# Optimization experiments

Measured on AMD Instinct MI355X. Metric: run time of the kernel, lower is better.

The kernel has to match this reference:

```python
import jax, jax.numpy as jnp
import numpy as np

NUM_NODES = 500000
INPUT_DIM = 256
ATTN_DIM = 64
NUM_GRAPHS = 512


def setup_inputs() -> dict:
    key = jax.random.key(0)
    ks = jax.random.split(key, 6)
    x = jax.random.normal(ks[0], (NUM_NODES, INPUT_DIM), dtype=jnp.float32)
    batch = jnp.sort(jax.random.randint(ks[1], (NUM_NODES,), 0, NUM_GRAPHS, dtype=jnp.int32)).astype(jnp.int64)
    # Xavier-uniform style init for linear weights, normal(0, 0.1) for context
    lim1 = float(np.sqrt(6.0 / (INPUT_DIM + ATTN_DIM)))
    W_att = jax.random.uniform(ks[2], (ATTN_DIM, INPUT_DIM), minval=-lim1, maxval=lim1, dtype=jnp.float32)
    b_att = jnp.zeros((ATTN_DIM,), dtype=jnp.float32)
    ctx = 0.1 * jax.random.normal(ks[3], (ATTN_DIM,), dtype=jnp.float32)
    lim2 = float(np.sqrt(6.0 / (INPUT_DIM + INPUT_DIM)))
    W_out = jax.random.uniform(ks[4], (INPUT_DIM, INPUT_DIM), minval=-lim2, maxval=lim2, dtype=jnp.float32)
    b_out = jnp.zeros((INPUT_DIM,), dtype=jnp.float32)
    return {"x": x, "batch": batch, "W_att": W_att, "b_att": b_att, "ctx": ctx, "W_out": W_out, "b_out": b_out}


def reference(x, batch, W_att, b_att, ctx, W_out, b_out):
    seg = batch.astype(jnp.int32)
    # attention scores per node: tanh(x W^T + b) . ctx  -> [N]
    logits = jnp.tanh(x @ W_att.T + b_att)
    scores = logits @ ctx  # [N]
    # segment-wise stable softmax
    seg_max = jax.ops.segment_max(scores, seg, num_segments=NUM_GRAPHS)
    exp_s = jnp.exp(scores - seg_max[seg])
    seg_sum = jax.ops.segment_sum(exp_s, seg, num_segments=NUM_GRAPHS)
    w = exp_s / (seg_sum[seg] + 1e-8)  # [N]
    # weighted segment-sum pooling -> [B, D]
    pooled = jax.ops.segment_sum(x * w[:, None], seg, num_segments=NUM_GRAPHS)
    return pooled @ W_out.T + b_out
```

## Files before the change

### kernel.cpp

```cpp
#include <hip/hip_runtime.h>
#include <hip/hip_bf16.h>
#include <math.h>

#define N_NODES 500000
#define DIM 256
#define ADIM 64
#define NG 512
#define PSPLIT 4

typedef __attribute__((ext_vector_type(8))) short short8;
typedef __attribute__((ext_vector_type(4))) short short4v;
typedef __attribute__((ext_vector_type(4))) float floatx4;

__device__ inline unsigned short f2bf(float f) {
    union { float f; unsigned int u; } v; v.f = f;
    unsigned int u = v.u;
    unsigned int r = u + 0x7FFFu + ((u >> 16) & 1u);
    return (unsigned short)(r >> 16);
}

__global__ __launch_bounds__(256) void k_prep(const float* __restrict__ W_out,
                                              float* __restrict__ Wt_out) {
    int idx = blockIdx.x * 256 + threadIdx.x;
    if (idx < DIM * DIM) {
        int o = idx / DIM, d = idx % DIM;
        Wt_out[d * DIM + o] = W_out[idx];
    }
}

__global__ __launch_bounds__(256) void k_offsets(const int* __restrict__ batch,
                                                 int* __restrict__ seg_start) {
    int i = blockIdx.x * 256 + threadIdx.x;
    if (i >= N_NODES) return;
    int b = batch[i];
    if (i == 0) {
        for (int g = 0; g <= b; g++) seg_start[g] = 0;
    } else {
        int pb = batch[i - 1];
        if (pb != b) {
            for (int g = pb + 1; g <= b; g++) seg_start[g] = i;
        }
    }
    if (i == N_NODES - 1) {
        for (int g = b + 1; g <= NG; g++) seg_start[g] = N_NODES;
    }
}

__global__ __launch_bounds__(256) void k_scores(const float* __restrict__ x,
                                                const float* __restrict__ W_att,
                                                const float* __restrict__ b_att,
                                                const float* __restrict__ ctx,
                                                float* __restrict__ scores) {
    __shared__ __align__(16) unsigned short xs[64 * 40];
    __shared__ float sacc[4][64];

    const int t = threadIdx.x;
    const int wave = t >> 6;
    const int lane = t & 63;
    const int quad = lane >> 4;
    const int lcol = lane & 15;
    const int base = blockIdx.x * 64;

    short8 bfrag[8];
    {
        const float* wr = W_att + (size_t)(16 * wave + lcol) * DIM + quad * 8;
#pragma unroll
        for (int s = 0; s < 8; s++) {
            float4 f0 = *(const float4*)(wr + s * 32);
            float4 f1 = *(const float4*)(wr + s * 32 + 4);
            short8 b;
            b[0] = (short)f2bf(f0.x); b[1] = (short)f2bf(f0.y);
            b[2] = (short)f2bf(f0.z); b[3] = (short)f2bf(f0.w);
            b[4] = (short)f2bf(f1.x); b[5] = (short)f2bf(f1.y);
            b[6] = (short)f2bf(f1.z); b[7] = (short)f2bf(f1.w);
            bfrag[s] = b;
        }
    }

    const int srow = t >> 2;
    const int sk = (t & 3) * 4;
    const int node_s = base + srow;
    const bool valid = node_s < N_NODES;
    const float* xrow = x + (size_t)node_s * DIM;

    floatx4 acc[4];
#pragma unroll
    for (int mt = 0; mt < 4; mt++) acc[mt] = (floatx4)0.f;

    float4 p0, p1;
    p0 = make_float4(0.f, 0.f, 0.f, 0.f); p1 = p0;
    if (valid) {
        p0 = *(const float4*)(xrow + sk);
        p1 = *(const float4*)(xrow + sk + 16);
    }

    for (int s = 0; s < 8; s++) {
        short4v w0, w1;
        w0[0] = (short)f2bf(p0.x); w0[1] = (short)f2bf(p0.y);
        w0[2] = (short)f2bf(p0.z); w0[3] = (short)f2bf(p0.w);
        w1[0] = (short)f2bf(p1.x); w1[1] = (short)f2bf(p1.y);
        w1[2] = (short)f2bf(p1.z); w1[3] = (short)f2bf(p1.w);
        *(short4v*)(xs + srow * 40 + sk) = w0;
        *(short4v*)(xs + srow * 40 + sk + 16) = w1;

        float4 n0 = make_float4(0.f, 0.f, 0.f, 0.f), n1 = n0;
        if (s < 7 && valid) {
            n0 = *(const float4*)(xrow + (s + 1) * 32 + sk);
            n1 = *(const float4*)(xrow + (s + 1) * 32 + sk + 16);
        }
        __syncthreads();

#pragma unroll
        for (int mt = 0; mt < 4; mt++) {
            short8 afrag = *(const short8*)(xs + (mt * 16 + lcol) * 40 + quad * 8);
            acc[mt] = __builtin_amdgcn_mfma_f32_16x16x32_bf16(afrag, bfrag[s], acc[mt], 0, 0, 0);
        }
        __syncthreads();
        p0 = n0; p1 = n1;
    }

    const float ctxv = ctx[16 * wave + lcol];
    const float bv = b_att[16 * wave + lcol];
    float partial[4][4];
#pragma unroll
    for (int mt = 0; mt < 4; mt++) {
#pragma unroll
        for (int r = 0; r < 4; r++) {
            float v = ctxv * tanhf(acc[mt][r] + bv);
            v += __shfl_xor(v, 1);
            v += __shfl_xor(v, 2);
            v += __shfl_xor(v, 4);
            v += __shfl_xor(v, 8);
            partial[mt][r] = v;
        }
    }
    if (lcol == 0) {
#pragma unroll
        for (int mt = 0; mt < 4; mt++)
#pragma unroll
            for (int r = 0; r < 4; r++)
                sacc[wave][mt * 16 + quad * 4 + r] = partial[mt][r];
    }
    __syncthreads();
    if (t < 64) {
        float sres = (sacc[0][t] + sacc[1][t]) + (sacc[2][t] + sacc[3][t]);
        int node = base + t;
        if (node < N_NODES) scores[node] = sres;
    }
}

__global__ __launch_bounds__(256) void k_segsoftmax(float* __restrict__ scores,
                                                    const int* __restrict__ seg_start) {
    int g = blockIdx.x;
    int s0 = seg_start[g], s1 = seg_start[g + 1];
    int t = threadIdx.x;
    __shared__ float red[256];

    float m = -INFINITY;
    for (int i = s0 + t; i < s1; i += 256) m = fmaxf(m, scores[i]);
    red[t] = m;
    __syncthreads();
    for (int off = 128; off > 0; off >>= 1) {
        if (t < off) red[t] = fmaxf(red[t], red[t + off]);
        __syncthreads();
    }
    m = red[0];
    __syncthreads();

    float sum = 0.f;
    for (int i = s0 + t; i < s1; i += 256) sum += __expf(scores[i] - m);
    red[t] = sum;
    __syncthreads();
    for (int off = 128; off > 0; off >>= 1) {
        if (t < off) red[t] += red[t + off];
        __syncthreads();
    }
    float inv = 1.f / (red[0] + 1e-8f);
    __syncthreads();

    for (int i = s0 + t; i < s1; i += 256) scores[i] = __expf(scores[i] - m) * inv;
}

__global__ __launch_bounds__(256) void k_pool(const float* __restrict__ x,
                                              const float* __restrict__ w,
                                              const int* __restrict__ seg_start,
                                              float* __restrict__ partial) {
    int g = blockIdx.x / PSPLIT, sp = blockIdx.x % PSPLIT;
    int s0 = seg_start[g], s1 = seg_start[g + 1];
    int len = s1 - s0;
    int chunk = (len + PSPLIT - 1) / PSPLIT;
    int c0 = s0 + sp * chunk;
    int c1 = min(s1, c0 + chunk);

    int t = threadIdx.x;
    int c = (t & 63) * 4;
    int grp = t >> 6;

    float4 acc = make_float4(0.f, 0.f, 0.f, 0.f);
    for (int i = c0 + grp; i < c1; i += 4) {
        float wi = w[i];
        float4 v = *(const float4*)(x + (size_t)i * DIM + c);
        acc.x += wi * v.x;
        acc.y += wi * v.y;
        acc.z += wi * v.z;
        acc.w += wi * v.w;
    }

    __shared__ float4 red[4][64];
    red[grp][t & 63] = acc;
    __syncthreads();
    if (t < 64) {
        float4 r0 = red[0][t], r1 = red[1][t], r2 = red[2][t], r3 = red[3][t];
        float4 r;
        r.x = (r0.x + r1.x) + (r2.x + r3.x);
        r.y = (r0.y + r1.y) + (r2.y + r3.y);
        r.z = (r0.z + r1.z) + (r2.z + r3.z);
        r.w = (r0.w + r1.w) + (r2.w + r3.w);
        *(float4*)(partial + (size_t)blockIdx.x * DIM + t * 4) = r;
    }
}

__global__ __launch_bounds__(256) void k_pool_reduce(const float* __restrict__ partial,
                                                     float* __restrict__ pooled) {
    int g = blockIdx.x;
    int t = threadIdx.x;
    float s = 0.f;
#pragma unroll
    for (int sp = 0; sp < PSPLIT; sp++)
        s += partial[(size_t)(g * PSPLIT + sp) * DIM + t];
    pooled[(size_t)g * DIM + t] = s;
}

__global__ __launch_bounds__(256) void k_out(const float* __restrict__ pooled,
                                             const float* __restrict__ WtOut,
                                             const float* __restrict__ b_out,
                                             float* __restrict__ out) {
    int g = blockIdx.x;
    int t = threadIdx.x;
    __shared__ float p[256];
    p[t] = pooled[g * DIM + t];
    __syncthreads();
    float acc = b_out[t];
#pragma unroll 4
    for (int d = 0; d < DIM; d++) acc += p[d] * WtOut[d * DIM + t];
    out[g * DIM + t] = acc;
}

extern "C" void kernel_launch(void* const* d_in, const int* in_sizes, int n_in,
                              void* d_out, int out_size, void* d_ws, size_t ws_size,
                              hipStream_t stream) {
    (void)in_sizes; (void)n_in; (void)out_size; (void)ws_size;
    const float* x     = (const float*)d_in[0];
    const int*   batch = (const int*)d_in[1];
    const float* W_att = (const float*)d_in[2];
    const float* b_att = (const float*)d_in[3];
    const float* ctx   = (const float*)d_in[4];
    const float* W_out = (const float*)d_in[5];
    const float* b_out = (const float*)d_in[6];
    float* out = (float*)d_out;

    float* scores  = (float*)d_ws;
    float* partial = scores + 500032;
    float* pooled  = partial + 524288;
    float* Wt_out  = pooled + 131072;
    int*   seg_start = (int*)(Wt_out + 65536);

    k_prep<<<dim3(DIM), dim3(256), 0, stream>>>(W_out, Wt_out);
    k_offsets<<<dim3((N_NODES + 255) / 256), dim3(256), 0, stream>>>(batch, seg_start);
    k_scores<<<dim3((N_NODES + 63) / 64), dim3(256), 0, stream>>>(x, W_att, b_att, ctx, scores);
    k_segsoftmax<<<dim3(NG), dim3(256), 0, stream>>>(scores, seg_start);
    k_pool<<<dim3(NG * PSPLIT), dim3(256), 0, stream>>>(x, scores, seg_start, partial);
    k_pool_reduce<<<dim3(NG), dim3(256), 0, stream>>>(partial, pooled);
    k_out<<<dim3(NG), dim3(256), 0, stream>>>(pooled, Wt_out, b_out, out);
}
```

Baseline: 800.0 us.

## Fuse scoring, segment softmax and pooling into one pass over x

Merges the score GEMM, segment softmax and weighted pooling into a single kernel, so x is read from global memory once instead of twice. The per-segment max is replaced by a fixed shift equal to sum|ctx|, which bounds the scores because tanh lies in [-1, 1]. Each block pools its bf16-staged x tile from LDS and atomically adds partial sums and exp-sums per graph; normalization moves into the output kernel. A cheaper tanh and preconverted bf16 W_att are added. The cost is bf16 precision in the pooled values, a different epsilon, and atomic contention on segment accumulators.

```diff
diff --git a/kernel.cpp b/kernel.cpp
--- a/kernel.cpp
+++ b/kernel.cpp
@@ -6,10 +6,9 @@
 #define DIM 256
 #define ADIM 64
 #define NG 512
-#define PSPLIT 4
+#define NBLK 7813
 
 typedef __attribute__((ext_vector_type(8))) short short8;
-typedef __attribute__((ext_vector_type(4))) short short4v;
 typedef __attribute__((ext_vector_type(4))) float floatx4;
 
 __device__ inline unsigned short f2bf(float f) {
@@ -19,40 +18,56 @@
     return (unsigned short)(r >> 16);
 }
 
+__device__ inline unsigned pk_bf2(float a, float b) {
+    __hip_bfloat162 h = __float22bfloat162_rn(make_float2(a, b));
+    union { __hip_bfloat162 h; unsigned u; } cv; cv.h = h;
+    return cv.u;
+}
+
+__device__ inline float tanh_fast(float xv) {
+    float e = __expf(2.0f * fabsf(xv));
+    float r = 1.0f - 2.0f * __builtin_amdgcn_rcpf(e + 1.0f);
+    return copysignf(r, xv);
+}
+
 __global__ __launch_bounds__(256) void k_prep(const float* __restrict__ W_out,
-                                              float* __restrict__ Wt_out) {
-    int idx = blockIdx.x * 256 + threadIdx.x;
-    if (idx < DIM * DIM) {
-        int o = idx / DIM, d = idx % DIM;
+                                              const float* __restrict__ W_att,
+                                              const float* __restrict__ ctx,
+                                              float* __restrict__ Wt_out,
+                                              unsigned short* __restrict__ Wbf,
+                                              float* __restrict__ cnorm,
+                                              float* __restrict__ zero_base) {
+    int b = blockIdx.x, t = threadIdx.x;
+    if (b < 256) {
+        int idx = b * 256 + t;
+        int o = idx >> 8, d = idx & 255;
         Wt_out[d * DIM + o] = W_out[idx];
-    }
-}
-
-__global__ __launch_bounds__(256) void k_offsets(const int* __restrict__ batch,
-                                                 int* __restrict__ seg_start) {
-    int i = blockIdx.x * 256 + threadIdx.x;
-    if (i >= N_NODES) return;
-    int b = batch[i];
-    if (i == 0) {
-        for (int g = 0; g <= b; g++) seg_start[g] = 0;
-    } else {
-        int pb = batch[i - 1];
-        if (pb != b) {
-            for (int g = pb + 1; g <= b; g++) seg_start[g] = i;
-        }
-    }
-    if (i == N_NODES - 1) {
-        for (int g = b + 1; g <= NG; g++) seg_start[g] = N_NODES;
-    }
-}
-
-__global__ __launch_bounds__(256) void k_scores(const float* __restrict__ x,
-                                                const float* __restrict__ W_att,
-                                                const float* __restrict__ b_att,
-                                                const float* __restrict__ ctx,
-                                                float* __restrict__ scores) {
-    __shared__ __align__(16) unsigned short xs[64 * 40];
+    } else if (b < 320) {
+        int idx = (b - 256) * 256 + t;
+        Wbf[idx] = f2bf(W_att[idx]);
+    } else if (b < 834) {
+        int idx = (b - 320) * 256 + t;
+        zero_base[idx] = 0.f;
+    } else if (t == 0) {
+        float s = 0.f;
+        for (int k = 0; k < ADIM; ++k) s += fabsf(ctx[k]);
+        *cnorm = s;
+    }
+}
+
+__global__ __launch_bounds__(256, 3) void k_fused(const float* __restrict__ x,
+                                                  const unsigned short* __restrict__ Wbf,
+                                                  const float* __restrict__ b_att,
+                                                  const float* __restrict__ ctx,
+                                                  const int* __restrict__ batch,
+                                                  const float* __restrict__ cnorm,
+                                                  float* __restrict__ accum,
+                                                  float* __restrict__ ssum) {
+    __shared__ __align__(16) unsigned short xs[8][65][40];
     __shared__ float sacc[4][64];
+    __shared__ float pbuf[64];
+    __shared__ int   gbuf[64];
+    __shared__ __align__(16) float redp[4][64][4];
 
     const int t = threadIdx.x;
     const int wave = t >> 6;
@@ -60,21 +75,13 @@
     const int quad = lane >> 4;
     const int lcol = lane & 15;
     const int base = blockIdx.x * 64;
+    const float cn = *cnorm;
 
     short8 bfrag[8];
     {
-        const float* wr = W_att + (size_t)(16 * wave + lcol) * DIM + quad * 8;
-#pragma unroll
-        for (int s = 0; s < 8; s++) {
-            float4 f0 = *(const float4*)(wr + s * 32);
-            float4 f1 = *(const float4*)(wr + s * 32 + 4);
-            short8 b;
-            b[0] = (short)f2bf(f0.x); b[1] = (short)f2bf(f0.y);
-            b[2] = (short)f2bf(f0.z); b[3] = (short)f2bf(f0.w);
-            b[4] = (short)f2bf(f1.x); b[5] = (short)f2bf(f1.y);
-            b[6] = (short)f2bf(f1.z); b[7] = (short)f2bf(f1.w);
-            bfrag[s] = b;
-        }
+        const unsigned short* wr = Wbf + (size_t)(16 * wave + lcol) * DIM + quad * 8;
+#pragma unroll
+        for (int s = 0; s < 8; ++s) bfrag[s] = *(const short8*)(wr + s * 32);
     }
 
     const int srow = t >> 2;
@@ -83,167 +90,112 @@
     const bool valid = node_s < N_NODES;
     const float* xrow = x + (size_t)node_s * DIM;
 
+    float4 h0[8], h1[8];
+#pragma unroll
+    for (int s = 0; s < 8; ++s) { h0[s] = make_float4(0.f, 0.f, 0.f, 0.f); h1[s] = h0[s]; }
+    if (valid) {
+#pragma unroll
+        for (int s = 0; s < 8; ++s) {
+            h0[s] = *(const float4*)(xrow + s * 32 + sk);
+            h1[s] = *(const float4*)(xrow + s * 32 + sk + 16);
+        }
+    }
+#pragma unroll
+    for (int s = 0; s < 8; ++s) {
+        uint2 w0, w1;
+        w0.x = pk_bf2(h0[s].x, h0[s].y); w0.y = pk_bf2(h0[s].z, h0[s].w);
+        w1.x = pk_bf2(h1[s].x, h1[s].y); w1.y = pk_bf2(h1[s].z, h1[s].w);
+        *(uint2*)&xs[s][srow][sk]      = w0;
+        *(uint2*)&xs[s][srow][sk + 16] = w1;
+    }
+    __syncthreads();
+
     floatx4 acc[4];
 #pragma unroll
-    for (int mt = 0; mt < 4; mt++) acc[mt] = (floatx4)0.f;
-
-    float4 p0, p1;
-    p0 = make_float4(0.f, 0.f, 0.f, 0.f); p1 = p0;
-    if (valid) {
-        p0 = *(const float4*)(xrow + sk);
-        p1 = *(const float4*)(xrow + sk + 16);
-    }
-
-    for (int s = 0; s < 8; s++) {
-        short4v w0, w1;
-        w0[0] = (short)f2bf(p0.x); w0[1] = (short)f2bf(p0.y);
-        w0[2] = (short)f2bf(p0.z); w0[3] = (short)f2bf(p0.w);
-        w1[0] = (short)f2bf(p1.x); w1[1] = (short)f2bf(p1.y);
-        w1[2] = (short)f2bf(p1.z); w1[3] = (short)f2bf(p1.w);
-        *(short4v*)(xs + srow * 40 + sk) = w0;
-        *(short4v*)(xs + srow * 40 + sk + 16) = w1;
-
-        float4 n0 = make_float4(0.f, 0.f, 0.f, 0.f), n1 = n0;
-        if (s < 7 && valid) {
-            n0 = *(const float4*)(xrow + (s + 1) * 32 + sk);
-            n1 = *(const float4*)(xrow + (s + 1) * 32 + sk + 16);
-        }
-        __syncthreads();
-
-#pragma unroll
-        for (int mt = 0; mt < 4; mt++) {
-            short8 afrag = *(const short8*)(xs + (mt * 16 + lcol) * 40 + quad * 8);
+    for (int mt = 0; mt < 4; ++mt) acc[mt] = (floatx4)0.f;
+#pragma unroll
+    for (int s = 0; s < 8; ++s) {
+#pragma unroll
+        for (int mt = 0; mt < 4; ++mt) {
+            short8 afrag = *(const short8*)&xs[s][mt * 16 + lcol][quad * 8];
             acc[mt] = __builtin_amdgcn_mfma_f32_16x16x32_bf16(afrag, bfrag[s], acc[mt], 0, 0, 0);
         }
-        __syncthreads();
-        p0 = n0; p1 = n1;
     }
 
     const float ctxv = ctx[16 * wave + lcol];
     const float bv = b_att[16 * wave + lcol];
-    float partial[4][4];
-#pragma unroll
-    for (int mt = 0; mt < 4; mt++) {
-#pragma unroll
-        for (int r = 0; r < 4; r++) {
-            float v = ctxv * tanhf(acc[mt][r] + bv);
+#pragma unroll
+    for (int mt = 0; mt < 4; ++mt) {
+#pragma unroll
+        for (int r = 0; r < 4; ++r) {
+            float v = ctxv * tanh_fast(acc[mt][r] + bv);
             v += __shfl_xor(v, 1);
             v += __shfl_xor(v, 2);
             v += __shfl_xor(v, 4);
             v += __shfl_xor(v, 8);
-            partial[mt][r] = v;
-        }
-    }
-    if (lcol == 0) {
-#pragma unroll
-        for (int mt = 0; mt < 4; mt++)
-#pragma unroll
-            for (int r = 0; r < 4; r++)
-                sacc[wave][mt * 16 + quad * 4 + r] = partial[mt][r];
+            if (lcol == 0) sacc[wave][mt * 16 + quad * 4 + r] = v;
+        }
     }
     __syncthreads();
     if (t < 64) {
         float sres = (sacc[0][t] + sacc[1][t]) + (sacc[2][t] + sacc[3][t]);
         int node = base + t;
-        if (node < N_NODES) scores[node] = sres;
-    }
-}
-
-__global__ __launch_bounds__(256) void k_segsoftmax(float* __restrict__ scores,
-                                                    const int* __restrict__ seg_start) {
-    int g = blockIdx.x;
-    int s0 = seg_start[g], s1 = seg_start[g + 1];
-    int t = threadIdx.x;
-    __shared__ float red[256];
-
-    float m = -INFINITY;
-    for (int i = s0 + t; i < s1; i += 256) m = fmaxf(m, scores[i]);
-    red[t] = m;
-    __syncthreads();
-    for (int off = 128; off > 0; off >>= 1) {
-        if (t < off) red[t] = fmaxf(red[t], red[t + off]);
+        bool v = node < N_NODES;
+        pbuf[t] = v ? __expf(sres - cn) : 0.f;
+        gbuf[t] = batch[v ? node : (N_NODES - 1)];
+    }
+    __syncthreads();
+
+    const int g0 = gbuf[0];
+    const int g1 = gbuf[63];
+    const int ps = lane >> 3;
+    const int pc = (lane & 7) * 4;
+    for (int g = g0; g <= g1; ++g) {
+        float4 a4 = make_float4(0.f, 0.f, 0.f, 0.f);
+#pragma unroll 4
+        for (int j = 0; j < 16; ++j) {
+            int i = (wave << 4) + j;
+            float wp = (gbuf[i] == g) ? pbuf[i] : 0.f;
+            if (wp != 0.f) {
+                uint2 v = *(const uint2*)&xs[ps][i][pc];
+                a4.x += wp * __uint_as_float(v.x << 16);
+                a4.y += wp * __uint_as_float(v.x & 0xffff0000u);
+                a4.z += wp * __uint_as_float(v.y << 16);
+                a4.w += wp * __uint_as_float(v.y & 0xffff0000u);
+            }
+        }
+        *(float4*)&redp[wave][lane][0] = a4;
+        float sp = 0.f;
+        if (t < 64) sp = (gbuf[t] == g) ? pbuf[t] : 0.f;
         __syncthreads();
-    }
-    m = red[0];
-    __syncthreads();
-
-    float sum = 0.f;
-    for (int i = s0 + t; i < s1; i += 256) sum += __expf(scores[i] - m);
-    red[t] = sum;
-    __syncthreads();
-    for (int off = 128; off > 0; off >>= 1) {
-        if (t < off) red[t] += red[t + off];
+        float r = ((redp[0][t >> 2][t & 3] + redp[1][t >> 2][t & 3]) +
+                   (redp[2][t >> 2][t & 3] + redp[3][t >> 2][t & 3]));
+        atomicAdd(&accum[(size_t)g * DIM + t], r);
+        if (t < 64) {
+            sp += __shfl_xor(sp, 1);  sp += __shfl_xor(sp, 2);
+            sp += __shfl_xor(sp, 4);  sp += __shfl_xor(sp, 8);
+            sp += __shfl_xor(sp, 16); sp += __shfl_xor(sp, 32);
+            if (t == 0) atomicAdd(&ssum[g], sp);
+        }
         __syncthreads();
     }
-    float inv = 1.f / (red[0] + 1e-8f);
-    __syncthreads();
-
-    for (int i = s0 + t; i < s1; i += 256) scores[i] = __expf(scores[i] - m) * inv;
-}
-
-__global__ __launch_bounds__(256) void k_pool(const float* __restrict__ x,
-                                              const float* __restrict__ w,
-                                              const int* __restrict__ seg_start,
-                                              float* __restrict__ partial) {
-    int g = blockIdx.x / PSPLIT, sp = blockIdx.x % PSPLIT;
-    int s0 = seg_start[g], s1 = seg_start[g + 1];
-    int len = s1 - s0;
-    int chunk = (len + PSPLIT - 1) / PSPLIT;
-    int c0 = s0 + sp * chunk;
-    int c1 = min(s1, c0 + chunk);
-
-    int t = threadIdx.x;
-    int c = (t & 63) * 4;
-    int grp = t >> 6;
-
-    float4 acc = make_float4(0.f, 0.f, 0.f, 0.f);
-    for (int i = c0 + grp; i < c1; i += 4) {
-        float wi = w[i];
-        float4 v = *(const float4*)(x + (size_t)i * DIM + c);
-        acc.x += wi * v.x;
-        acc.y += wi * v.y;
-        acc.z += wi * v.z;
-        acc.w += wi * v.w;
-    }
-
-    __shared__ float4 red[4][64];
-    red[grp][t & 63] = acc;
-    __syncthreads();
-    if (t < 64) {
-        float4 r0 = red[0][t], r1 = red[1][t], r2 = red[2][t], r3 = red[3][t];
-        float4 r;
-        r.x = (r0.x + r1.x) + (r2.x + r3.x);
-        r.y = (r0.y + r1.y) + (r2.y + r3.y);
-        r.z = (r0.z + r1.z) + (r2.z + r3.z);
-        r.w = (r0.w + r1.w) + (r2.w + r3.w);
-        *(float4*)(partial + (size_t)blockIdx.x * DIM + t * 4) = r;
-    }
-}
-
-__global__ __launch_bounds__(256) void k_pool_reduce(const float* __restrict__ partial,
-                                                     float* __restrict__ pooled) {
-    int g = blockIdx.x;
-    int t = threadIdx.x;
-    float s = 0.f;
-#pragma unroll
-    for (int sp = 0; sp < PSPLIT; sp++)
-        s += partial[(size_t)(g * PSPLIT + sp) * DIM + t];
-    pooled[(size_t)g * DIM + t] = s;
-}
-
-__global__ __launch_bounds__(256) void k_out(const float* __restrict__ pooled,
+}
+
+__global__ __launch_bounds__(256) void k_out(const float* __restrict__ accum,
+                                             const float* __restrict__ ssum,
                                              const float* __restrict__ WtOut,
                                              const float* __restrict__ b_out,
                                              float* __restrict__ out) {
     int g = blockIdx.x;
     int t = threadIdx.x;
-    __shared__ float p[256];
-    p[t] = pooled[g * DIM + t];
+    __shared__ float pl[256];
+    float inv = 1.0f / (ssum[g] + 1e-20f);
+    pl[t] = accum[(size_t)g * DIM + t] * inv;
     __syncthreads();
     float acc = b_out[t];
 #pragma unroll 4
-    for (int d = 0; d < DIM; d++) acc += p[d] * WtOut[d * DIM + t];
-    out[g * DIM + t] = acc;
+    for (int d = 0; d < DIM; ++d) acc += pl[d] * WtOut[d * DIM + t];
+    out[(size_t)g * DIM + t] = acc;
 }
 
 extern "C" void kernel_launch(void* const* d_in, const int* in_sizes, int n_in,
@@ -259,17 +211,13 @@
     const float* b_out = (const float*)d_in[6];
     float* out = (float*)d_out;
 
-    float* scores  = (float*)d_ws;
-    float* partial = scores + 500032;
-    float* pooled  = partial + 524288;
-    float* Wt_out  = pooled + 131072;
-    int*   seg_start = (int*)(Wt_out + 65536);
-
-    k_prep<<<dim3(DIM), dim3(256), 0, stream>>>(W_out, Wt_out);
-    k_offsets<<<dim3((N_NODES + 255) / 256), dim3(256), 0, stream>>>(batch, seg_start);
-    k_scores<<<dim3((N_NODES + 63) / 64), dim3(256), 0, stream>>>(x, W_att, b_att, ctx, scores);
-    k_segsoftmax<<<dim3(NG), dim3(256), 0, stream>>>(scores, seg_start);
-    k_pool<<<dim3(NG * PSPLIT), dim3(256), 0, stream>>>(x, scores, seg_start, partial);
-    k_pool_reduce<<<dim3(NG), dim3(256), 0, stream>>>(partial, pooled);
-    k_out<<<dim3(NG), dim3(256), 0, stream>>>(pooled, Wt_out, b_out, out);
-}
+    float* accum = (float*)d_ws;
+    float* ssum  = accum + 131072;
+    float* Wt    = ssum + 512;
+    unsigned short* Wbf = (unsigned short*)(Wt + 65536);
+    float* cnorm = (float*)(Wbf + 16384);
+
+    k_prep<<<dim3(835), dim3(256), 0, stream>>>(W_out, W_att, ctx, Wt, Wbf, cnorm, accum);
+    k_fused<<<dim3(NBLK), dim3(256), 0, stream>>>(x, Wbf, b_att, ctx, batch, cnorm, accum, ssum);
+    k_out<<<dim3(NG), dim3(256), 0, stream>>>(accum, ssum, Wt, b_out, out);
+}
```

Result: faster. 698.0 us (-12.7%).
